# Performance work log

Measured on AMD Instinct MI355X. Metric: run time of the kernel, lower is better.

The kernel has to match this reference:

```python
import jax, jax.numpy as jnp
import numpy as np

DIM = 2048
HEADS = 16
HEAD_DIM = 128
B = 2
T = 2048


def _rope_as_in_source(x):
    # x: (b, h, t, d). FAITHFUL to the source bug: RotaryEmbedding uses
    # x.shape[1] (the HEADS axis, since it is called after transpose) as the
    # 'sequence' index, so rotation angle depends on head index and is
    # broadcast over the true sequence axis.
    n = x.shape[1]  # == heads
    d = x.shape[-1]
    inv_freq = 1.0 / (10000.0 ** (jnp.arange(0, d, 2, dtype=jnp.float32) / d))
    freqs = jnp.arange(n, dtype=jnp.float32)[:, None] * inv_freq[None, :]  # (h, d/2)
    cos = jnp.cos(freqs)[None, :, None, :]  # (1, h, 1, d/2)
    sin = jnp.sin(freqs)[None, :, None, :]
    x1 = x[..., 0::2]
    x2 = x[..., 1::2]
    out = jnp.stack([x1 * cos - x2 * sin, x1 * sin + x2 * cos], axis=-1)
    return out.reshape(x.shape)


def setup_inputs() -> dict:
    key = jax.random.key(0)
    ks = jax.random.split(key, 9)
    s_in = 1.0 / np.sqrt(DIM)
    hd = HEADS * HEAD_DIM
    s_o = 1.0 / np.sqrt(hd)
    return {
        "x": jax.random.normal(ks[0], (B, T, DIM), dtype=jnp.float32),
        "Wq": jax.random.normal(ks[1], (DIM, hd), dtype=jnp.float32) * s_in,
        "bq": jnp.zeros((hd,), dtype=jnp.float32),
        "Wk": jax.random.normal(ks[2], (DIM, hd), dtype=jnp.float32) * s_in,
        "bk": jnp.zeros((hd,), dtype=jnp.float32),
        "Wv": jax.random.normal(ks[3], (DIM, hd), dtype=jnp.float32) * s_in,
        "bv": jnp.zeros((hd,), dtype=jnp.float32),
        "Wo": jax.random.normal(ks[4], (hd, DIM), dtype=jnp.float32) * s_o,
        "bo": jnp.zeros((DIM,), dtype=jnp.float32),
    }


def reference(x, Wq, bq, Wk, bk, Wv, bv, Wo, bo):
    b, t, c = x.shape
    q = (x @ Wq + bq).reshape(b, t, HEADS, HEAD_DIM).transpose(0, 2, 1, 3)
    k = (x @ Wk + bk).reshape(b, t, HEADS, HEAD_DIM).transpose(0, 2, 1, 3)
    v = (x @ Wv + bv).reshape(b, t, HEADS, HEAD_DIM).transpose(0, 2, 1, 3)
    q = _rope_as_in_source(q)
    k = _rope_as_in_source(k)
    scale = 1.0 / np.sqrt(HEAD_DIM)
    scores = jnp.einsum("bhqd,bhkd->bhqk", q, k) * scale  # (b,h,t,t)
    attn = jax.nn.softmax(scores, axis=-1)
    out = jnp.einsum("bhqk,bhkd->bhqd", attn, v)  # (b,h,t,d)
    out = out.transpose(0, 2, 1, 3).reshape(b, t, HEADS * HEAD_DIM)
    return out @ Wo + bo
```

## Files before the change

kernel.cpp:

```cpp
#include <hip/hip_runtime.h>

typedef unsigned short ushort_t;
typedef unsigned int uint_t;
typedef __attribute__((ext_vector_type(8))) short short8;
typedef __attribute__((ext_vector_type(4))) float f32x4;
typedef __attribute__((ext_vector_type(4))) unsigned short ushort4_t;
typedef __attribute__((ext_vector_type(4))) unsigned int uint4_t;

__device__ inline float b2f(ushort_t u) {
    unsigned int x = ((unsigned int)u) << 16;
    return __builtin_bit_cast(float, x);
}
__device__ inline ushort_t f2b(float f) {
    unsigned int x = __builtin_bit_cast(unsigned int, f);
    x += 0x7fffu + ((x >> 16) & 1u);
    return (ushort_t)(x >> 16);
}
__device__ inline uint_t cvt_pk_bf16(float lo, float hi) {
    uint_t r;
    asm("v_cvt_pk_bf16_f32 %0, %1, %2" : "=v"(r) : "v"(lo), "v"(hi));
    return r;
}

__device__ inline void gload16(const void* g, void* l) {
    __builtin_amdgcn_global_load_lds(
        (const __attribute__((address_space(1))) void*)g,
        (__attribute__((address_space(3))) void*)l, 16, 0, 0);
}

__global__ __launch_bounds__(256)
void cast_bf16(const float* __restrict__ src, ushort_t* __restrict__ dst) {
    size_t i = ((size_t)blockIdx.x * 256 + threadIdx.x) * 8;
    f32x4 a = *reinterpret_cast<const f32x4*>(src + i);
    f32x4 b = *reinterpret_cast<const f32x4*>(src + i + 4);
    short8 v;
#pragma unroll
    for (int j = 0; j < 4; ++j) { v[j] = (short)f2b(a[j]); v[4 + j] = (short)f2b(b[j]); }
    *reinterpret_cast<short8*>(dst + i) = v;
}

template <typename ST>
__global__ __launch_bounds__(64)
void transp(const ST* __restrict__ src, ushort_t* __restrict__ dst, int R, int C) {
    src += (size_t)blockIdx.z * R * C;
    dst += (size_t)blockIdx.z * R * C;
    int r0 = blockIdx.x * 64 + ((threadIdx.x >> 3) << 3);
    int c0 = blockIdx.y * 64 + ((threadIdx.x & 7) << 3);
    ushort_t v[8][8];
#pragma unroll
    for (int i = 0; i < 8; ++i) {
        const ST* p = src + (size_t)(r0 + i) * C + c0;
        if constexpr (sizeof(ST) == 4) {
            f32x4 a = *reinterpret_cast<const f32x4*>(p);
            f32x4 b = *reinterpret_cast<const f32x4*>(p + 4);
#pragma unroll
            for (int j = 0; j < 4; ++j) { v[i][j] = f2b(a[j]); v[i][4 + j] = f2b(b[j]); }
        } else {
            short8 a = *reinterpret_cast<const short8*>(p);
#pragma unroll
            for (int j = 0; j < 8; ++j) v[i][j] = (ushort_t)a[j];
        }
    }
#pragma unroll
    for (int c = 0; c < 8; ++c) {
        short8 w;
#pragma unroll
        for (int i = 0; i < 8; ++i) w[i] = (short)v[i][c];
        *reinterpret_cast<short8*>(dst + (size_t)(c0 + c) * R + r0) = w;
    }
}

template <bool BHTD, bool ROPE>
__global__ __launch_bounds__(256)
void gemm_bt(const ushort_t* __restrict__ A, const ushort_t* __restrict__ Bt,
             const float* __restrict__ bias, void* __restrict__ Cv,
             int M, int N, int K, float oscale) {
    __shared__ __align__(16) ushort_t As[128 * 64];
    __shared__ __align__(16) ushort_t Bs[128 * 64];
    const int tid = threadIdx.x, lane = tid & 63, wid = tid >> 6;
    const int l15 = lane & 15, g = lane >> 4;
    const int wr = wid >> 1, wc = wid & 1;
    const int m0 = blockIdx.y * 128, n0 = blockIdx.x * 128;
    f32x4 acc[4][4] = {};
    for (int k0 = 0; k0 < K; k0 += 64) {
#pragma unroll
        for (int is = 0; is < 4; ++is) {
            int c = is * 256 + tid;
            int row = c >> 3, sub = c & 7;
            int ks = (sub ^ (row & 7)) << 3;
            char* ldst = (char*)As + (size_t)(is * 256 + wid * 64) * 16;
            gload16(A + (size_t)(m0 + row) * K + k0 + ks, ldst);
            char* ldstB = (char*)Bs + (size_t)(is * 256 + wid * 64) * 16;
            gload16(Bt + (size_t)(n0 + row) * K + k0 + ks, ldstB);
        }
        __syncthreads();
#pragma unroll
        for (int kk = 0; kk < 2; ++kk) {
            short8 af[4], bf[4];
#pragma unroll
            for (int i = 0; i < 4; ++i) {
                int ra = wr * 64 + i * 16 + l15;
                af[i] = *reinterpret_cast<const short8*>(
                    (const char*)As + ra * 128 + (((4 * kk + g) ^ (ra & 7)) << 4));
                int rb = wc * 64 + i * 16 + l15;
                bf[i] = *reinterpret_cast<const short8*>(
                    (const char*)Bs + rb * 128 + (((4 * kk + g) ^ (rb & 7)) << 4));
            }
#pragma unroll
            for (int i = 0; i < 4; ++i)
#pragma unroll
                for (int j = 0; j < 4; ++j)
                    acc[i][j] = __builtin_amdgcn_mfma_f32_16x16x32_bf16(af[i], bf[j], acc[i][j], 0, 0, 0);
        }
        __syncthreads();
    }
#pragma unroll
    for (int j = 0; j < 4; ++j) {
        int n = n0 + wc * 64 + j * 16 + l15;
        float bj = bias[n];
        float sn = 0.f, cs = 1.f, sgn = 0.f;
        if (ROPE) {
            int d = n & 127, h = (n >> 7) & 15;
            float inv = expf(-(float)(d >> 1) * (9.210340371976184f / 64.0f));
            sincosf((float)h * inv, &sn, &cs);
            sgn = (d & 1) ? sn : -sn;
        }
#pragma unroll
        for (int i = 0; i < 4; ++i) {
            int mbase = m0 + wr * 64 + i * 16 + g * 4;
#pragma unroll
            for (int r = 0; r < 4; ++r) {
                int m = mbase + r;
                float v = acc[i][j][r] + bj;
                if (ROPE) {
                    float p = __shfl_xor(v, 1, 64);
                    v = fmaf(p, sgn, v * cs);
                    v *= oscale;
                }
                if (BHTD) {
                    size_t addr = ((size_t)((m >> 11) * 16 + (n >> 7)) * 2048 + (m & 2047)) * 128 + (n & 127);
                    ((ushort_t*)Cv)[addr] = f2b(v);
                } else {
                    ((float*)Cv)[(size_t)m * N + n] = v;
                }
            }
        }
    }
}

__global__ __launch_bounds__(512)
void fattn(const ushort_t* __restrict__ Q, const ushort_t* __restrict__ K,
           const ushort_t* __restrict__ Vt, ushort_t* __restrict__ O) {
    __shared__ __align__(16) ushort_t Ks[2][64 * 128];
    __shared__ __align__(16) ushort_t Vs[2][128 * 64];
    const int tid = threadIdx.x, lane = tid & 63, wid = tid >> 6;
    const int l15 = lane & 15, g = lane >> 4;
    const int h = blockIdx.y, b = blockIdx.z;
    const size_t base = ((size_t)b * 16 + h) * (2048 * 128);
    const int q0 = blockIdx.x * 128 + wid * 16;
    short8 qf[4];
#pragma unroll
    for (int c = 0; c < 4; ++c)
        qf[c] = *reinterpret_cast<const short8*>(Q + base + (size_t)(q0 + l15) * 128 + c * 32 + g * 8);
    f32x4 oacc[8] = {};
    float m_r = -__builtin_inff(), l_r = 0.f;
    const int addrA = ((32 * (g & 1)) + l15) << 2;
    const int addrB = addrA + 64;
    const bool hi = (lane & 32) != 0;

    auto stage = [&](int kv0, int bsel) {
#pragma unroll
        for (int is = 0; is < 2; ++is) {
            {
                int c = is * 512 + tid;
                int row = c >> 4, sub = c & 15;
                int dsrc = (sub ^ (row & 7)) << 3;
                gload16(K + base + (size_t)(kv0 + row) * 128 + dsrc,
                        (char*)Ks[bsel] + (size_t)c * 16);
            }
            {
                int c = is * 512 + tid;
                int row = c >> 3, sub = c & 7;
                int tsrc = (sub ^ (row & 7)) << 3;
                gload16(Vt + base + (size_t)row * 2048 + kv0 + tsrc,
                        (char*)Vs[bsel] + (size_t)c * 16);
            }
        }
    };

    stage(0, 0);
    asm volatile("s_waitcnt vmcnt(0)" ::: "memory");
    __builtin_amdgcn_s_barrier();

    for (int it = 0; it < 32; ++it) {
        const int cur = it & 1;
        if (it < 31) stage((it + 1) << 6, cur ^ 1);
        f32x4 s[4] = {};
        __builtin_amdgcn_s_setprio(1);
#pragma unroll
        for (int nt = 0; nt < 4; ++nt) {
            int kvr = nt * 16 + l15;
#pragma unroll
            for (int c = 0; c < 4; ++c) {
                short8 kf = *reinterpret_cast<const short8*>(
                    (const char*)Ks[cur] + kvr * 256 + (((4 * c + g) ^ (kvr & 7)) << 4));
                s[nt] = __builtin_amdgcn_mfma_f32_16x16x32_bf16(kf, qf[c], s[nt], 0, 0, 0);
            }
        }
        __builtin_amdgcn_s_setprio(0);
        float pm = fmaxf(fmaxf(fmaxf(s[0][0], s[0][1]), fmaxf(s[0][2], s[0][3])),
                         fmaxf(fmaxf(s[1][0], s[1][1]), fmaxf(s[1][2], s[1][3])));
        pm = fmaxf(pm, fmaxf(fmaxf(fmaxf(s[2][0], s[2][1]), fmaxf(s[2][2], s[2][3])),
                             fmaxf(fmaxf(s[3][0], s[3][1]), fmaxf(s[3][2], s[3][3]))));
        pm = fmaxf(pm, __shfl_xor(pm, 16, 64));
        pm = fmaxf(pm, __shfl_xor(pm, 32, 64));
        if (!__all(pm <= m_r + 5.0f)) {
            float mn = fmaxf(m_r, pm);
            float fac = exp2f(m_r - mn);
            m_r = mn;
            l_r *= fac;
#pragma unroll
            for (int nt2 = 0; nt2 < 8; ++nt2)
#pragma unroll
                for (int r = 0; r < 4; ++r) oacc[nt2][r] *= fac;
        }
        uint_t W[4][2];
        float rs = 0.f;
#pragma unroll
        for (int nt = 0; nt < 4; ++nt) {
            float p0 = exp2f(s[nt][0] - m_r);
            float p1 = exp2f(s[nt][1] - m_r);
            float p2 = exp2f(s[nt][2] - m_r);
            float p3 = exp2f(s[nt][3] - m_r);
            rs += (p0 + p1) + (p2 + p3);
            W[nt][0] = cvt_pk_bf16(p0, p1);
            W[nt][1] = cvt_pk_bf16(p2, p3);
        }
        rs += __shfl_xor(rs, 16, 64);
        rs += __shfl_xor(rs, 32, 64);
        l_r += rs;
        __builtin_amdgcn_s_setprio(1);
#pragma unroll
        for (int ks = 0; ks < 2; ++ks) {
            uint_t xa, xb, w0, w1, w2, w3;
            xa = (uint_t)__builtin_amdgcn_ds_bpermute(addrA, (int)W[2 * ks][0]);
            xb = (uint_t)__builtin_amdgcn_ds_bpermute(addrA, (int)W[2 * ks + 1][0]);
            w0 = hi ? xb : xa;
            xa = (uint_t)__builtin_amdgcn_ds_bpermute(addrA, (int)W[2 * ks][1]);
            xb = (uint_t)__builtin_amdgcn_ds_bpermute(addrA, (int)W[2 * ks + 1][1]);
            w1 = hi ? xb : xa;
            xa = (uint_t)__builtin_amdgcn_ds_bpermute(addrB, (int)W[2 * ks][0]);
            xb = (uint_t)__builtin_amdgcn_ds_bpermute(addrB, (int)W[2 * ks + 1][0]);
            w2 = hi ? xb : xa;
            xa = (uint_t)__builtin_amdgcn_ds_bpermute(addrB, (int)W[2 * ks][1]);
            xb = (uint_t)__builtin_amdgcn_ds_bpermute(addrB, (int)W[2 * ks + 1][1]);
            w3 = hi ? xb : xa;
            uint4_t wv; wv[0] = w0; wv[1] = w1; wv[2] = w2; wv[3] = w3;
            short8 pb = __builtin_bit_cast(short8, wv);
#pragma unroll
            for (int nt2 = 0; nt2 < 8; ++nt2) {
                int dr = nt2 * 16 + l15;
                short8 vb = *reinterpret_cast<const short8*>(
                    (const char*)Vs[cur] + dr * 128 + (((ks * 4 + g) ^ (dr & 7)) << 4));
                oacc[nt2] = __builtin_amdgcn_mfma_f32_16x16x32_bf16(vb, pb, oacc[nt2], 0, 0, 0);
            }
        }
        __builtin_amdgcn_s_setprio(0);
        asm volatile("s_waitcnt vmcnt(0)" ::: "memory");
        __builtin_amdgcn_s_barrier();
    }
    float inv = 1.f / l_r;
    const size_t orow = ((size_t)b * 2048 + q0 + l15) * 2048 + (size_t)h * 128;
#pragma unroll
    for (int nt2 = 0; nt2 < 8; ++nt2) {
        ushort4_t w;
#pragma unroll
        for (int r = 0; r < 4; ++r) w[r] = f2b(oacc[nt2][r] * inv);
        *reinterpret_cast<ushort4_t*>(O + orow + nt2 * 16 + g * 4) = w;
    }
}

extern "C" void kernel_launch(void* const* d_in, const int* in_sizes, int n_in,
                              void* d_out, int out_size, void* d_ws, size_t ws_size,
                              hipStream_t stream) {
    const float* x  = (const float*)d_in[0];
    const float* Wq = (const float*)d_in[1];
    const float* bq = (const float*)d_in[2];
    const float* Wk = (const float*)d_in[3];
    const float* bk = (const float*)d_in[4];
    const float* Wv = (const float*)d_in[5];
    const float* bv = (const float*)d_in[6];
    const float* Wo = (const float*)d_in[7];
    const float* bo = (const float*)d_in[8];
    float* out = (float*)d_out;
    ushort_t* ws  = (ushort_t*)d_ws;

    const size_t WSZ = 2048ull * 2048;
    const size_t TSZ = 2ull * 16 * 2048 * 128;
    ushort_t* xb  = ws;
    ushort_t* Wtq = xb + TSZ;
    ushort_t* Wtk = Wtq + WSZ;
    ushort_t* Wtv = Wtk + WSZ;
    ushort_t* Wto = Wtv + WSZ;
    ushort_t* Qb  = Wto + WSZ;
    ushort_t* Kb  = Qb + TSZ;
    ushort_t* Vtb = Kb + TSZ;
    ushort_t* Sb  = Vtb + TSZ;

    const float QSC = 0.08838834764831845f * 1.4426950408889634f;

    cast_bf16<<<dim3(4096), 256, 0, stream>>>(x, xb);
    transp<float><<<dim3(32, 32, 1), 64, 0, stream>>>(Wq, Wtq, 2048, 2048);
    transp<float><<<dim3(32, 32, 1), 64, 0, stream>>>(Wk, Wtk, 2048, 2048);
    transp<float><<<dim3(32, 32, 1), 64, 0, stream>>>(Wv, Wtv, 2048, 2048);
    transp<float><<<dim3(32, 32, 1), 64, 0, stream>>>(Wo, Wto, 2048, 2048);

    gemm_bt<true, true ><<<dim3(16, 32), 256, 0, stream>>>(xb, Wtq, bq, Qb, 4096, 2048, 2048, QSC);
    gemm_bt<true, true ><<<dim3(16, 32), 256, 0, stream>>>(xb, Wtk, bk, Kb, 4096, 2048, 2048, 1.0f);
    gemm_bt<true, false><<<dim3(16, 32), 256, 0, stream>>>(xb, Wtv, bv, Sb, 4096, 2048, 2048, 1.0f);

    transp<ushort_t><<<dim3(32, 2, 32), 64, 0, stream>>>(Sb, Vtb, 2048, 128);

    fattn<<<dim3(16, 16, 2), 512, 0, stream>>>(Qb, Kb, Vtb, Sb);

    gemm_bt<false, false><<<dim3(16, 32), 256, 0, stream>>>(Sb, Wto, bo, out, 4096, 2048, 2048, 1.0f);
}
```

Before: 326.8 us.

## Double-buffer GEMM LDS tiles and widen blocks to 128x256 with 8 waves

The projection GEMM now uses 512-thread blocks computing 128x256 tiles with 8 waves in a 2x4 arrangement, and double-buffers the A and B LDS tiles so the next K-slice loads while the current one is multiplied. It also raises wave priority around the MFMA bursts. The goal is to hide global-load latency behind compute and halve block count per GEMM. The cost is 96KB of LDS per block, which can limit occupancy, and fewer blocks (256) per GEMM on a device with many CUs.

```diff
diff --git a/kernel.cpp b/kernel.cpp
--- a/kernel.cpp
+++ b/kernel.cpp
@@ -71,29 +71,43 @@
 }
 
 template <bool BHTD, bool ROPE>
-__global__ __launch_bounds__(256)
+__global__ __launch_bounds__(512, 2)
 void gemm_bt(const ushort_t* __restrict__ A, const ushort_t* __restrict__ Bt,
              const float* __restrict__ bias, void* __restrict__ Cv,
              int M, int N, int K, float oscale) {
-    __shared__ __align__(16) ushort_t As[128 * 64];
-    __shared__ __align__(16) ushort_t Bs[128 * 64];
+    __shared__ __align__(16) ushort_t As[2][128 * 64];
+    __shared__ __align__(16) ushort_t Bs[2][256 * 64];
     const int tid = threadIdx.x, lane = tid & 63, wid = tid >> 6;
     const int l15 = lane & 15, g = lane >> 4;
-    const int wr = wid >> 1, wc = wid & 1;
-    const int m0 = blockIdx.y * 128, n0 = blockIdx.x * 128;
+    const int wr = wid >> 2, wc = wid & 3;
+    const int m0 = blockIdx.y * 128, n0 = blockIdx.x * 256;
     f32x4 acc[4][4] = {};
-    for (int k0 = 0; k0 < K; k0 += 64) {
-#pragma unroll
-        for (int is = 0; is < 4; ++is) {
-            int c = is * 256 + tid;
+
+    auto stage = [&](int k0, int bsel) {
+#pragma unroll
+        for (int is = 0; is < 2; ++is) {
+            int c = is * 512 + tid;
             int row = c >> 3, sub = c & 7;
             int ks = (sub ^ (row & 7)) << 3;
-            char* ldst = (char*)As + (size_t)(is * 256 + wid * 64) * 16;
-            gload16(A + (size_t)(m0 + row) * K + k0 + ks, ldst);
-            char* ldstB = (char*)Bs + (size_t)(is * 256 + wid * 64) * 16;
-            gload16(Bt + (size_t)(n0 + row) * K + k0 + ks, ldstB);
-        }
-        __syncthreads();
+            gload16(A + (size_t)(m0 + row) * K + k0 + ks, (char*)As[bsel] + (size_t)c * 16);
+        }
+#pragma unroll
+        for (int is = 0; is < 4; ++is) {
+            int c = is * 512 + tid;
+            int row = c >> 3, sub = c & 7;
+            int ks = (sub ^ (row & 7)) << 3;
+            gload16(Bt + (size_t)(n0 + row) * K + k0 + ks, (char*)Bs[bsel] + (size_t)c * 16);
+        }
+    };
+
+    stage(0, 0);
+    asm volatile("s_waitcnt vmcnt(0)" ::: "memory");
+    __builtin_amdgcn_s_barrier();
+
+    const int NT = K >> 6;
+    for (int kt = 0; kt < NT; ++kt) {
+        const int cur = kt & 1;
+        if (kt < NT - 1) stage((kt + 1) << 6, cur ^ 1);
 #pragma unroll
         for (int kk = 0; kk < 2; ++kk) {
             short8 af[4], bf[4];
@@ -101,18 +115,21 @@
             for (int i = 0; i < 4; ++i) {
                 int ra = wr * 64 + i * 16 + l15;
                 af[i] = *reinterpret_cast<const short8*>(
-                    (const char*)As + ra * 128 + (((4 * kk + g) ^ (ra & 7)) << 4));
+                    (const char*)As[cur] + ra * 128 + (((4 * kk + g) ^ (ra & 7)) << 4));
                 int rb = wc * 64 + i * 16 + l15;
                 bf[i] = *reinterpret_cast<const short8*>(
-                    (const char*)Bs + rb * 128 + (((4 * kk + g) ^ (rb & 7)) << 4));
-            }
+                    (const char*)Bs[cur] + rb * 128 + (((4 * kk + g) ^ (rb & 7)) << 4));
+            }
+            __builtin_amdgcn_s_setprio(1);
 #pragma unroll
             for (int i = 0; i < 4; ++i)
 #pragma unroll
                 for (int j = 0; j < 4; ++j)
                     acc[i][j] = __builtin_amdgcn_mfma_f32_16x16x32_bf16(af[i], bf[j], acc[i][j], 0, 0, 0);
-        }
-        __syncthreads();
+            __builtin_amdgcn_s_setprio(0);
+        }
+        asm volatile("s_waitcnt vmcnt(0)" ::: "memory");
+        __builtin_amdgcn_s_barrier();
     }
 #pragma unroll
     for (int j = 0; j < 4; ++j) {
@@ -315,13 +332,13 @@
     transp<float><<<dim3(32, 32, 1), 64, 0, stream>>>(Wv, Wtv, 2048, 2048);
     transp<float><<<dim3(32, 32, 1), 64, 0, stream>>>(Wo, Wto, 2048, 2048);
 
-    gemm_bt<true, true ><<<dim3(16, 32), 256, 0, stream>>>(xb, Wtq, bq, Qb, 4096, 2048, 2048, QSC);
-    gemm_bt<true, true ><<<dim3(16, 32), 256, 0, stream>>>(xb, Wtk, bk, Kb, 4096, 2048, 2048, 1.0f);
-    gemm_bt<true, false><<<dim3(16, 32), 256, 0, stream>>>(xb, Wtv, bv, Sb, 4096, 2048, 2048, 1.0f);
+    gemm_bt<true, true ><<<dim3(8, 32), 512, 0, stream>>>(xb, Wtq, bq, Qb, 4096, 2048, 2048, QSC);
+    gemm_bt<true, true ><<<dim3(8, 32), 512, 0, stream>>>(xb, Wtk, bk, Kb, 4096, 2048, 2048, 1.0f);
+    gemm_bt<true, false><<<dim3(8, 32), 512, 0, stream>>>(xb, Wtv, bv, Sb, 4096, 2048, 2048, 1.0f);
 
     transp<ushort_t><<<dim3(32, 2, 32), 64, 0, stream>>>(Sb, Vtb, 2048, 128);
 
     fattn<<<dim3(16, 16, 2), 512, 0, stream>>>(Qb, Kb, Vtb, Sb);
 
-    gemm_bt<false, false><<<dim3(16, 32), 256, 0, stream>>>(Sb, Wto, bo, out, 4096, 2048, 2048, 1.0f);
-}
+    gemm_bt<false, false><<<dim3(8, 32), 512, 0, stream>>>(Sb, Wto, bo, out, 4096, 2048, 2048, 1.0f);
+}
```

Result: slower. 356.8 us (+9.2%).

## Switch flash attention to 32x32x16 MFMA with 32-row waves and permlane swap

Applied to the files above, without the earlier changes.

Rewrites the attention kernel so each of 4 waves handles 32 query rows using 32x32x16 bf16 MFMA instead of 16x16x32 with 8 waves of 16 rows. Probabilities are repacked into the B operand with v_permlane32_swap instead of many ds_bpermute ops, and K/V fragment reuse per wave doubles. Block size drops to 256 threads, so fewer waves share the same LDS tiles, with more accumulator registers per wave and lower occupancy as the risk.

```diff
diff --git a/kernel.cpp b/kernel.cpp
--- a/kernel.cpp
+++ b/kernel.cpp
@@ -4,6 +4,7 @@
 typedef unsigned int uint_t;
 typedef __attribute__((ext_vector_type(8))) short short8;
 typedef __attribute__((ext_vector_type(4))) float f32x4;
+typedef __attribute__((ext_vector_type(16))) float f32x16;
 typedef __attribute__((ext_vector_type(4))) unsigned short ushort4_t;
 typedef __attribute__((ext_vector_type(4))) unsigned int uint4_t;
 
@@ -148,38 +149,35 @@
     }
 }
 
-__global__ __launch_bounds__(512)
+__global__ __launch_bounds__(256)
 void fattn(const ushort_t* __restrict__ Q, const ushort_t* __restrict__ K,
            const ushort_t* __restrict__ Vt, ushort_t* __restrict__ O) {
     __shared__ __align__(16) ushort_t Ks[2][64 * 128];
     __shared__ __align__(16) ushort_t Vs[2][128 * 64];
     const int tid = threadIdx.x, lane = tid & 63, wid = tid >> 6;
-    const int l15 = lane & 15, g = lane >> 4;
-    const int h = blockIdx.y, b = blockIdx.z;
-    const size_t base = ((size_t)b * 16 + h) * (2048 * 128);
-    const int q0 = blockIdx.x * 128 + wid * 16;
-    short8 qf[4];
-#pragma unroll
-    for (int c = 0; c < 4; ++c)
-        qf[c] = *reinterpret_cast<const short8*>(Q + base + (size_t)(q0 + l15) * 128 + c * 32 + g * 8);
-    f32x4 oacc[8] = {};
+    const int l31 = lane & 31, hl = lane >> 5;
+    const int hd = blockIdx.y, b = blockIdx.z;
+    const size_t base = ((size_t)b * 16 + hd) * (2048 * 128);
+    const int q0 = blockIdx.x * 128 + wid * 32;
+    short8 qf[8];
+#pragma unroll
+    for (int kc = 0; kc < 8; ++kc)
+        qf[kc] = *reinterpret_cast<const short8*>(Q + base + (size_t)(q0 + l31) * 128 + kc * 16 + hl * 8);
+    f32x16 oacc[4] = {};
     float m_r = -__builtin_inff(), l_r = 0.f;
-    const int addrA = ((32 * (g & 1)) + l15) << 2;
-    const int addrB = addrA + 64;
-    const bool hi = (lane & 32) != 0;
 
     auto stage = [&](int kv0, int bsel) {
 #pragma unroll
-        for (int is = 0; is < 2; ++is) {
+        for (int is = 0; is < 4; ++is) {
             {
-                int c = is * 512 + tid;
+                int c = is * 256 + tid;
                 int row = c >> 4, sub = c & 15;
                 int dsrc = (sub ^ (row & 7)) << 3;
                 gload16(K + base + (size_t)(kv0 + row) * 128 + dsrc,
                         (char*)Ks[bsel] + (size_t)c * 16);
             }
             {
-                int c = is * 512 + tid;
+                int c = is * 256 + tid;
                 int row = c >> 3, sub = c & 7;
                 int tsrc = (sub ^ (row & 7)) << 3;
                 gload16(Vt + base + (size_t)row * 2048 + kv0 + tsrc,
@@ -195,24 +193,22 @@
     for (int it = 0; it < 32; ++it) {
         const int cur = it & 1;
         if (it < 31) stage((it + 1) << 6, cur ^ 1);
-        f32x4 s[4] = {};
+        f32x16 s0 = {}, s1 = {};
         __builtin_amdgcn_s_setprio(1);
 #pragma unroll
-        for (int nt = 0; nt < 4; ++nt) {
-            int kvr = nt * 16 + l15;
-#pragma unroll
-            for (int c = 0; c < 4; ++c) {
-                short8 kf = *reinterpret_cast<const short8*>(
-                    (const char*)Ks[cur] + kvr * 256 + (((4 * c + g) ^ (kvr & 7)) << 4));
-                s[nt] = __builtin_amdgcn_mfma_f32_16x16x32_bf16(kf, qf[c], s[nt], 0, 0, 0);
-            }
+        for (int kc = 0; kc < 8; ++kc) {
+            int sw = ((2 * kc + hl) ^ (l31 & 7)) << 4;
+            short8 kf0 = *reinterpret_cast<const short8*>((const char*)Ks[cur] + l31 * 256 + sw);
+            s0 = __builtin_amdgcn_mfma_f32_32x32x16_bf16(kf0, qf[kc], s0, 0, 0, 0);
+            short8 kf1 = *reinterpret_cast<const short8*>((const char*)Ks[cur] + (32 + l31) * 256 + sw);
+            s1 = __builtin_amdgcn_mfma_f32_32x32x16_bf16(kf1, qf[kc], s1, 0, 0, 0);
         }
         __builtin_amdgcn_s_setprio(0);
-        float pm = fmaxf(fmaxf(fmaxf(s[0][0], s[0][1]), fmaxf(s[0][2], s[0][3])),
-                         fmaxf(fmaxf(s[1][0], s[1][1]), fmaxf(s[1][2], s[1][3])));
-        pm = fmaxf(pm, fmaxf(fmaxf(fmaxf(s[2][0], s[2][1]), fmaxf(s[2][2], s[2][3])),
-                             fmaxf(fmaxf(s[3][0], s[3][1]), fmaxf(s[3][2], s[3][3]))));
-        pm = fmaxf(pm, __shfl_xor(pm, 16, 64));
+        float pm = fmaxf(s0[0], s0[1]);
+#pragma unroll
+        for (int r = 2; r < 16; ++r) pm = fmaxf(pm, s0[r]);
+#pragma unroll
+        for (int r = 0; r < 16; ++r) pm = fmaxf(pm, s1[r]);
         pm = fmaxf(pm, __shfl_xor(pm, 32, 64));
         if (!__all(pm <= m_r + 5.0f)) {
             float mn = fmaxf(m_r, pm);
@@ -220,49 +216,43 @@
             m_r = mn;
             l_r *= fac;
 #pragma unroll
-            for (int nt2 = 0; nt2 < 8; ++nt2)
-#pragma unroll
-                for (int r = 0; r < 4; ++r) oacc[nt2][r] *= fac;
-        }
-        uint_t W[4][2];
+            for (int dt = 0; dt < 4; ++dt)
+#pragma unroll
+                for (int r = 0; r < 16; ++r) oacc[dt][r] *= fac;
+        }
         float rs = 0.f;
 #pragma unroll
-        for (int nt = 0; nt < 4; ++nt) {
-            float p0 = exp2f(s[nt][0] - m_r);
-            float p1 = exp2f(s[nt][1] - m_r);
-            float p2 = exp2f(s[nt][2] - m_r);
-            float p3 = exp2f(s[nt][3] - m_r);
-            rs += (p0 + p1) + (p2 + p3);
-            W[nt][0] = cvt_pk_bf16(p0, p1);
-            W[nt][1] = cvt_pk_bf16(p2, p3);
-        }
-        rs += __shfl_xor(rs, 16, 64);
+        for (int r = 0; r < 16; ++r) { s0[r] = exp2f(s0[r] - m_r); rs += s0[r]; }
+#pragma unroll
+        for (int r = 0; r < 16; ++r) { s1[r] = exp2f(s1[r] - m_r); rs += s1[r]; }
         rs += __shfl_xor(rs, 32, 64);
         l_r += rs;
         __builtin_amdgcn_s_setprio(1);
 #pragma unroll
-        for (int ks = 0; ks < 2; ++ks) {
-            uint_t xa, xb, w0, w1, w2, w3;
-            xa = (uint_t)__builtin_amdgcn_ds_bpermute(addrA, (int)W[2 * ks][0]);
-            xb = (uint_t)__builtin_amdgcn_ds_bpermute(addrA, (int)W[2 * ks + 1][0]);
-            w0 = hi ? xb : xa;
-            xa = (uint_t)__builtin_amdgcn_ds_bpermute(addrA, (int)W[2 * ks][1]);
-            xb = (uint_t)__builtin_amdgcn_ds_bpermute(addrA, (int)W[2 * ks + 1][1]);
-            w1 = hi ? xb : xa;
-            xa = (uint_t)__builtin_amdgcn_ds_bpermute(addrB, (int)W[2 * ks][0]);
-            xb = (uint_t)__builtin_amdgcn_ds_bpermute(addrB, (int)W[2 * ks + 1][0]);
-            w2 = hi ? xb : xa;
-            xa = (uint_t)__builtin_amdgcn_ds_bpermute(addrB, (int)W[2 * ks][1]);
-            xb = (uint_t)__builtin_amdgcn_ds_bpermute(addrB, (int)W[2 * ks + 1][1]);
-            w3 = hi ? xb : xa;
-            uint4_t wv; wv[0] = w0; wv[1] = w1; wv[2] = w2; wv[3] = w3;
+        for (int c = 0; c < 4; ++c) {
+            const int cc = c & 1;
+            uint_t X0, X1, Y0, Y1;
+            if (c < 2) {
+                X0 = cvt_pk_bf16(s0[8 * cc + 0], s0[8 * cc + 1]);
+                X1 = cvt_pk_bf16(s0[8 * cc + 2], s0[8 * cc + 3]);
+                Y0 = cvt_pk_bf16(s0[8 * cc + 4], s0[8 * cc + 5]);
+                Y1 = cvt_pk_bf16(s0[8 * cc + 6], s0[8 * cc + 7]);
+            } else {
+                X0 = cvt_pk_bf16(s1[8 * cc + 0], s1[8 * cc + 1]);
+                X1 = cvt_pk_bf16(s1[8 * cc + 2], s1[8 * cc + 3]);
+                Y0 = cvt_pk_bf16(s1[8 * cc + 4], s1[8 * cc + 5]);
+                Y1 = cvt_pk_bf16(s1[8 * cc + 6], s1[8 * cc + 7]);
+            }
+            asm("v_permlane32_swap_b32 %0, %1" : "+v"(X0), "+v"(Y0));
+            asm("v_permlane32_swap_b32 %0, %1" : "+v"(X1), "+v"(Y1));
+            uint4_t wv; wv[0] = X0; wv[1] = X1; wv[2] = Y0; wv[3] = Y1;
             short8 pb = __builtin_bit_cast(short8, wv);
 #pragma unroll
-            for (int nt2 = 0; nt2 < 8; ++nt2) {
-                int dr = nt2 * 16 + l15;
-                short8 vb = *reinterpret_cast<const short8*>(
-                    (const char*)Vs[cur] + dr * 128 + (((ks * 4 + g) ^ (dr & 7)) << 4));
-                oacc[nt2] = __builtin_amdgcn_mfma_f32_16x16x32_bf16(vb, pb, oacc[nt2], 0, 0, 0);
+            for (int dt = 0; dt < 4; ++dt) {
+                int dr = dt * 32 + l31;
+                short8 vf = *reinterpret_cast<const short8*>(
+                    (const char*)Vs[cur] + dr * 128 + (((2 * c + hl) ^ (l31 & 7)) << 4));
+                oacc[dt] = __builtin_amdgcn_mfma_f32_32x32x16_bf16(vf, pb, oacc[dt], 0, 0, 0);
             }
         }
         __builtin_amdgcn_s_setprio(0);
@@ -270,13 +260,16 @@
         __builtin_amdgcn_s_barrier();
     }
     float inv = 1.f / l_r;
-    const size_t orow = ((size_t)b * 2048 + q0 + l15) * 2048 + (size_t)h * 128;
-#pragma unroll
-    for (int nt2 = 0; nt2 < 8; ++nt2) {
-        ushort4_t w;
-#pragma unroll
-        for (int r = 0; r < 4; ++r) w[r] = f2b(oacc[nt2][r] * inv);
-        *reinterpret_cast<ushort4_t*>(O + orow + nt2 * 16 + g * 4) = w;
+    const size_t orow = ((size_t)b * 2048 + q0 + l31) * 2048 + (size_t)hd * 128;
+#pragma unroll
+    for (int dt = 0; dt < 4; ++dt) {
+#pragma unroll
+        for (int m = 0; m < 4; ++m) {
+            ushort4_t w;
+#pragma unroll
+            for (int i = 0; i < 4; ++i) w[i] = f2b(oacc[dt][4 * m + i] * inv);
+            *reinterpret_cast<ushort4_t*>(O + orow + dt * 32 + m * 8 + hl * 4) = w;
+        }
     }
 }
 
@@ -321,7 +314,7 @@
 
     transp<ushort_t><<<dim3(32, 2, 32), 64, 0, stream>>>(Sb, Vtb, 2048, 128);
 
-    fattn<<<dim3(16, 16, 2), 512, 0, stream>>>(Qb, Kb, Vtb, Sb);
+    fattn<<<dim3(16, 16, 2), 256, 0, stream>>>(Qb, Kb, Vtb, Sb);
 
     gemm_bt<false, false><<<dim3(16, 32), 256, 0, stream>>>(Sb, Wto, bo, out, 4096, 2048, 2048, 1.0f);
 }
```

New measurement: 356.1 us. +9.0%, slower.
